# Kernel tuning notes

Measured on AMD Instinct MI355X. Metric: run time of the kernel, lower is better.

## Reference

```python
import jax, jax.numpy as jnp
import numpy as np

D_MODEL = 1024
NUM_HEADS = 16
DEPTH = D_MODEL // NUM_HEADS


def setup_inputs() -> dict:
    key = jax.random.key(0)
    ks = jax.random.split(key, 5)
    B, S = 2, 2048
    scale = 1.0 / np.sqrt(D_MODEL)
    x = jax.random.normal(ks[0], (B, S, D_MODEL), dtype=jnp.float32)
    wq = jax.random.normal(ks[1], (D_MODEL, D_MODEL), dtype=jnp.float32) * scale
    wk = jax.random.normal(ks[2], (D_MODEL, D_MODEL), dtype=jnp.float32) * scale
    wv = jax.random.normal(ks[3], (D_MODEL, D_MODEL), dtype=jnp.float32) * scale
    wo = jax.random.normal(ks[4], (D_MODEL, D_MODEL), dtype=jnp.float32) * scale
    zb = jnp.zeros((D_MODEL,), dtype=jnp.float32)
    return {"x": x, "wq": wq, "bq": zb, "wk": wk, "bk": zb, "wv": wv, "bv": zb, "wo": wo, "bo": zb}


def _split_heads(t):
    # [B, S, D] -> [B, H, S, depth]
    B, S, _ = t.shape
    return t.reshape(B, S, NUM_HEADS, DEPTH).transpose(0, 2, 1, 3)


def reference(x, wq, bq, wk, bk, wv, bv, wo, bo):
    q = _split_heads(x @ wq + bq)
    k = _split_heads(x @ wk + bk)
    v = _split_heads(x @ wv + bv)
    scores = jnp.einsum("bhqd,bhkd->bhqk", q, k) / jnp.sqrt(jnp.float32(DEPTH))
    attn = jax.nn.softmax(scores, axis=-1)
    out = jnp.einsum("bhqk,bhkd->bhqd", attn, v)  # [B, H, S, depth]
    B, H, S, d = out.shape
    out = out.transpose(0, 2, 1, 3).reshape(B, S, D_MODEL)
    return out @ wo + bo
```

## Files before the change

### kernel.cpp

```cpp
#include <hip/hip_runtime.h>
#include <stdint.h>

#define SS 2048
#define DM 1024
#define HD 16
#define DP 64
#define BB 2

#define QSCALE 0.18033688011112042f

typedef unsigned short u16;
typedef short bf16x8 __attribute__((ext_vector_type(8)));
typedef float f32x4 __attribute__((ext_vector_type(4)));

#if __has_builtin(__builtin_amdgcn_exp2f)
#define EXP2F __builtin_amdgcn_exp2f
#else
#define EXP2F exp2f
#endif

__device__ __forceinline__ u16 f2b(float f) {
  unsigned u = __builtin_bit_cast(unsigned, f);
  u = (u + 0x7fffu + ((u >> 16) & 1u)) >> 16;
  return (u16)u;
}

__device__ __forceinline__ void gl_lds16(const void* g, void* l) {
  __builtin_amdgcn_global_load_lds(
      (const __attribute__((address_space(1))) unsigned int*)g,
      (__attribute__((address_space(3))) unsigned int*)l, 16, 0, 0);
}

__global__ __launch_bounds__(256) void cast_bf16_kernel(const float* __restrict__ in,
                                                        u16* __restrict__ out, int n) {
  int i = (blockIdx.x * 256 + threadIdx.x) * 4;
  if (i + 3 < n) {
    float4 f = *reinterpret_cast<const float4*>(in + i);
    ushort4 o;
    o.x = f2b(f.x); o.y = f2b(f.y); o.z = f2b(f.z); o.w = f2b(f.w);
    *reinterpret_cast<ushort4*>(out + i) = o;
  }
}

__global__ __launch_bounds__(256) void tcast_kernel(const float* __restrict__ in,
                                                    u16* __restrict__ out, float scale) {
  __shared__ float tile[32][33];
  int tx = threadIdx.x & 31, ty = threadIdx.x >> 5;
  int c0 = blockIdx.x * 32;
  int r0 = blockIdx.y * 32;
#pragma unroll
  for (int j = 0; j < 4; ++j)
    tile[ty + j * 8][tx] = in[(size_t)(r0 + ty + j * 8) * DM + c0 + tx];
  __syncthreads();
#pragma unroll
  for (int j = 0; j < 4; ++j)
    out[(size_t)(c0 + ty + j * 8) * DM + r0 + tx] = f2b(tile[tx][ty + j * 8] * scale);
}

__global__ __launch_bounds__(256) void gemm_qkv(
    const u16* __restrict__ A, const u16* __restrict__ BT,
    const float* __restrict__ b0, const float* __restrict__ b1, const float* __restrict__ b2,
    u16* __restrict__ Oq, u16* __restrict__ Ok, u16* __restrict__ Ovt, int M, int K) {
  __shared__ __align__(16) u16 As[128][32];
  __shared__ __align__(16) u16 Bs[128][32];
  const int t = threadIdx.x;
  const int w = t >> 6, l = t & 63;
  const int lr = l & 15, lg = l >> 4;
  const int wr = w >> 1, wc = w & 1;
  const int m0 = blockIdx.y * 128, n0 = blockIdx.x * 128;

  const u16* Ab = A + (size_t)m0 * K;
  const u16* Bb = BT + (size_t)n0 * K;
  const int arow = t >> 2, achk = (t & 3) * 8;

  f32x4 acc[4][4];
#pragma unroll
  for (int mi = 0; mi < 4; ++mi)
#pragma unroll
    for (int ni = 0; ni < 4; ++ni)
      acc[mi][ni] = (f32x4){0.f, 0.f, 0.f, 0.f};

  char* AsB = (char*)(&As[0][0]);
  char* BsB = (char*)(&Bs[0][0]);

  for (int k0 = 0; k0 < K; k0 += 32) {
    gl_lds16(Ab + (size_t)arow * K + k0 + achk, AsB + t * 16);
    gl_lds16(Ab + (size_t)(arow + 64) * K + k0 + achk, AsB + t * 16 + 4096);
    gl_lds16(Bb + (size_t)arow * K + k0 + achk, BsB + t * 16);
    gl_lds16(Bb + (size_t)(arow + 64) * K + k0 + achk, BsB + t * 16 + 4096);
    __syncthreads();
    bf16x8 af[4], bfr[4];
#pragma unroll
    for (int mi = 0; mi < 4; ++mi)
      af[mi] = *(const bf16x8*)&As[wr * 64 + mi * 16 + lr][lg * 8];
#pragma unroll
    for (int ni = 0; ni < 4; ++ni)
      bfr[ni] = *(const bf16x8*)&Bs[wc * 64 + ni * 16 + lr][lg * 8];
#pragma unroll
    for (int mi = 0; mi < 4; ++mi)
#pragma unroll
      for (int ni = 0; ni < 4; ++ni)
        acc[mi][ni] =
            __builtin_amdgcn_mfma_f32_16x16x32_bf16(af[mi], bfr[ni], acc[mi][ni], 0, 0, 0);
    __syncthreads();
  }

  const int proj = n0 >> 10;
  const float* bias = proj == 0 ? b0 : (proj == 1 ? b1 : b2);
  const float bsc = proj == 0 ? QSCALE : 1.f;
  const int nloc0 = n0 & 1023;
#pragma unroll
  for (int mi = 0; mi < 4; ++mi)
#pragma unroll
    for (int ni = 0; ni < 4; ++ni)
#pragma unroll
      for (int i = 0; i < 4; ++i) {
        int gm = m0 + wr * 64 + mi * 16 + lg * 4 + i;
        int gn = nloc0 + wc * 64 + ni * 16 + lr;
        float vv = acc[mi][ni][i] + bias[gn] * bsc;
        int s = gm & (SS - 1), b = gm >> 11;
        int h = gn >> 6, d = gn & 63;
        if (proj == 2) {
          Ovt[(((size_t)(b * HD + h)) * DP + d) * SS + s] = f2b(vv);
        } else {
          u16* Op = proj == 0 ? Oq : Ok;
          Op[(((size_t)(b * HD + h)) * SS + s) * DP + d] = f2b(vv);
        }
      }
}

__global__ __launch_bounds__(256) void gemm_out(
    const u16* __restrict__ A, const u16* __restrict__ BT, const float* __restrict__ b0,
    float* __restrict__ FO, int M, int K) {
  __shared__ __align__(16) u16 As[64][64];
  __shared__ __align__(16) u16 Bs[64][64];
  const int t = threadIdx.x;
  const int w = t >> 6, l = t & 63;
  const int lr = l & 15, lg = l >> 4;
  const int wr = w >> 1, wc = w & 1;
  const int m0 = blockIdx.y * 64, n0 = blockIdx.x * 64;

  const u16* Ab = A + (size_t)m0 * K;
  const u16* Bb = BT + (size_t)n0 * K;
  const int srow = t >> 3;
  const int gchk = ((t & 7) ^ (srow & 7)) * 8;

  f32x4 acc[2][2];
#pragma unroll
  for (int mi = 0; mi < 2; ++mi)
#pragma unroll
    for (int ni = 0; ni < 2; ++ni)
      acc[mi][ni] = (f32x4){0.f, 0.f, 0.f, 0.f};

  char* AsB = (char*)(&As[0][0]);
  char* BsB = (char*)(&Bs[0][0]);

  for (int k0 = 0; k0 < K; k0 += 64) {
    gl_lds16(Ab + (size_t)srow * K + k0 + gchk, AsB + t * 16);
    gl_lds16(Ab + (size_t)(srow + 32) * K + k0 + gchk, AsB + t * 16 + 4096);
    gl_lds16(Bb + (size_t)srow * K + k0 + gchk, BsB + t * 16);
    gl_lds16(Bb + (size_t)(srow + 32) * K + k0 + gchk, BsB + t * 16 + 4096);
    __syncthreads();
    bf16x8 af[2][2], bfr[2][2];
#pragma unroll
    for (int mi = 0; mi < 2; ++mi) {
      int r = wr * 32 + mi * 16 + lr;
#pragma unroll
      for (int kk = 0; kk < 2; ++kk)
        af[mi][kk] = *(const bf16x8*)&As[r][(((kk * 4 + lg) ^ (r & 7)) * 8)];
    }
#pragma unroll
    for (int ni = 0; ni < 2; ++ni) {
      int r = wc * 32 + ni * 16 + lr;
#pragma unroll
      for (int kk = 0; kk < 2; ++kk)
        bfr[ni][kk] = *(const bf16x8*)&Bs[r][(((kk * 4 + lg) ^ (r & 7)) * 8)];
    }
#pragma unroll
    for (int mi = 0; mi < 2; ++mi)
#pragma unroll
      for (int ni = 0; ni < 2; ++ni)
#pragma unroll
        for (int kk = 0; kk < 2; ++kk)
          acc[mi][ni] =
              __builtin_amdgcn_mfma_f32_16x16x32_bf16(af[mi][kk], bfr[ni][kk], acc[mi][ni], 0, 0, 0);
    __syncthreads();
  }

#pragma unroll
  for (int mi = 0; mi < 2; ++mi)
#pragma unroll
    for (int ni = 0; ni < 2; ++ni)
#pragma unroll
      for (int i = 0; i < 4; ++i) {
        int gm = m0 + wr * 32 + mi * 16 + lg * 4 + i;
        int gn = n0 + wc * 32 + ni * 16 + lr;
        FO[(size_t)gm * DM + gn] = acc[mi][ni][i] + b0[gn];
      }
}

__global__ __launch_bounds__(256) void attn_kernel(const u16* __restrict__ Q,
                                                   const u16* __restrict__ K,
                                                   const u16* __restrict__ VT,
                                                   u16* __restrict__ O) {
  __shared__ __align__(16) u16 Ks[64 * 64];
  __shared__ __align__(16) u16 Vs[64 * 64];
  __shared__ __align__(16) u16 Ps[4][16][68];
  const int t = threadIdx.x, w = t >> 6, l = t & 63;
  const int lr = l & 15, lg = l >> 4;
  const int bh = blockIdx.y;
  const int q0 = blockIdx.x * 64;
  const u16* Qb = Q + (size_t)bh * SS * DP;
  const u16* Kb = K + (size_t)bh * SS * DP;
  const u16* Vb = VT + (size_t)bh * DP * SS;

  const int qrow = q0 + w * 16 + lr;
  bf16x8 qf[2];
  qf[0] = *(const bf16x8*)(Qb + (size_t)qrow * DP + lg * 8);
  qf[1] = *(const bf16x8*)(Qb + (size_t)qrow * DP + 32 + lg * 8);

  bf16x8 ones8;
#pragma unroll
  for (int j = 0; j < 8; ++j) ones8[j] = (short)0x3f80;

  f32x4 oacc[4];
  f32x4 lac = (f32x4){0.f, 0.f, 0.f, 0.f};
#pragma unroll
  for (int i = 0; i < 4; ++i) oacc[i] = (f32x4){0.f, 0.f, 0.f, 0.f};

  const int srow = t >> 3;
  const int sswz = ((t & 7) ^ (srow & 7)) * 8;
  char* KsB = (char*)Ks;
  char* VsB = (char*)Vs;

  for (int t0 = 0; t0 < SS; t0 += 64) {
    gl_lds16(Kb + (size_t)(t0 + srow) * DP + sswz, KsB + t * 16);
    gl_lds16(Kb + (size_t)(t0 + srow + 32) * DP + sswz, KsB + t * 16 + 4096);
    gl_lds16(Vb + (size_t)srow * SS + t0 + sswz, VsB + t * 16);
    gl_lds16(Vb + (size_t)(srow + 32) * SS + t0 + sswz, VsB + t * 16 + 4096);
    __syncthreads();

    f32x4 sc[4];
#pragma unroll
    for (int n = 0; n < 4; ++n) sc[n] = (f32x4){0.f, 0.f, 0.f, 0.f};
#pragma unroll
    for (int n = 0; n < 4; ++n) {
      int r = n * 16 + lr;
#pragma unroll
      for (int kk = 0; kk < 2; ++kk) {
        int chk = ((kk * 4 + lg) ^ (r & 7)) * 8;
        bf16x8 bk8 = *(const bf16x8*)(Ks + r * 64 + chk);
        sc[n] = __builtin_amdgcn_mfma_f32_16x16x32_bf16(qf[kk], bk8, sc[n], 0, 0, 0);
      }
    }

#pragma unroll
    for (int n = 0; n < 4; ++n)
#pragma unroll
      for (int i = 0; i < 4; ++i)
        Ps[w][lg * 4 + i][n * 16 + lr] = f2b(EXP2F(sc[n][i]));
    asm volatile("s_waitcnt lgkmcnt(0)" ::: "memory");
    bf16x8 pf[2];
    pf[0] = *(const bf16x8*)&Ps[w][lr][lg * 8];
    pf[1] = *(const bf16x8*)&Ps[w][lr][32 + lg * 8];

#pragma unroll
    for (int kk = 0; kk < 2; ++kk)
      lac = __builtin_amdgcn_mfma_f32_16x16x32_bf16(pf[kk], ones8, lac, 0, 0, 0);

#pragma unroll
    for (int n = 0; n < 4; ++n) {
      int r = n * 16 + lr;
#pragma unroll
      for (int kk = 0; kk < 2; ++kk) {
        int chk = ((kk * 4 + lg) ^ (r & 7)) * 8;
        bf16x8 bv8 = *(const bf16x8*)(Vs + r * 64 + chk);
        oacc[n] = __builtin_amdgcn_mfma_f32_16x16x32_bf16(pf[kk], bv8, oacc[n], 0, 0, 0);
      }
    }
    __syncthreads();
  }

  const int b = bh >> 4, h = bh & 15;
  float inv[4];
#pragma unroll
  for (int i = 0; i < 4; ++i) inv[i] = 1.0f / lac[i];
#pragma unroll
  for (int n = 0; n < 4; ++n)
#pragma unroll
    for (int i = 0; i < 4; ++i) {
      int row = q0 + w * 16 + lg * 4 + i;
      int col = h * 64 + n * 16 + lr;
      O[((size_t)(b * SS + row)) * DM + col] = f2b(oacc[n][i] * inv[i]);
    }
}

extern "C" void kernel_launch(void* const* d_in, const int* in_sizes, int n_in,
                              void* d_out, int out_size, void* d_ws, size_t ws_size,
                              hipStream_t stream) {
  const float* x = (const float*)d_in[0];
  const float* wq = (const float*)d_in[1];
  const float* bq = (const float*)d_in[2];
  const float* wk = (const float*)d_in[3];
  const float* bk = (const float*)d_in[4];
  const float* wv = (const float*)d_in[5];
  const float* bv = (const float*)d_in[6];
  const float* wo = (const float*)d_in[7];
  const float* bo = (const float*)d_in[8];
  float* out = (float*)d_out;

  u16* ws = (u16*)d_ws;
  u16* xb = ws;
  u16* wt3 = ws + 4194304;
  u16* wot = ws + 7340032;
  u16* q = ws + 8388608;
  u16* k = ws + 12582912;
  u16* vt = ws + 16777216;
  u16* o = ws;

  cast_bf16_kernel<<<4096, 256, 0, stream>>>(x, xb, 4194304);
  tcast_kernel<<<dim3(32, 32), 256, 0, stream>>>(wq, wt3, QSCALE);
  tcast_kernel<<<dim3(32, 32), 256, 0, stream>>>(wk, wt3 + 1048576, 1.f);
  tcast_kernel<<<dim3(32, 32), 256, 0, stream>>>(wv, wt3 + 2097152, 1.f);
  tcast_kernel<<<dim3(32, 32), 256, 0, stream>>>(wo, wot, 1.f);

  gemm_qkv<<<dim3(24, 32), 256, 0, stream>>>(xb, wt3, bq, bk, bv, q, k, vt, 4096, 1024);
  attn_kernel<<<dim3(32, 32), 256, 0, stream>>>(q, k, vt, o);
  gemm_out<<<dim3(16, 64), 256, 0, stream>>>(o, wot, bo, out, 4096, 1024);
}
```

Baseline: 220.0 us.

## Double-buffer attention K/V tiles, enlarge tiles, vectorize V stores, merge weight casts

The attention kernel now runs 512 threads per block over 128 query rows and double-buffers the K/V LDS tiles, so the next tile loads while the current one is computed and each K/V tile is shared by more query rows. The output GEMM moves to 128x64 tiles so each B fragment serves more rows. The QKV epilogue writes the transposed V output as packed 4-element stores instead of scalar stores. The four weight transpose-casts become a single launch. The risks are higher register and LDS pressure per block, fewer blocks for the output GEMM, and an explicit vmcnt wait each iteration that may limit how much loading overlaps with compute.

```diff
diff --git a/kernel.cpp b/kernel.cpp
--- a/kernel.cpp
+++ b/kernel.cpp
@@ -42,9 +42,15 @@
   }
 }
 
-__global__ __launch_bounds__(256) void tcast_kernel(const float* __restrict__ in,
-                                                    u16* __restrict__ out, float scale) {
+__global__ __launch_bounds__(256) void tcast4_kernel(
+    const float* __restrict__ w0, const float* __restrict__ w1,
+    const float* __restrict__ w2, const float* __restrict__ w3,
+    u16* __restrict__ o0, u16* __restrict__ o1, u16* __restrict__ o2, u16* __restrict__ o3) {
   __shared__ float tile[32][33];
+  const int z = blockIdx.z;
+  const float* in = z == 0 ? w0 : (z == 1 ? w1 : (z == 2 ? w2 : w3));
+  u16* out = z == 0 ? o0 : (z == 1 ? o1 : (z == 2 ? o2 : o3));
+  const float scale = z == 0 ? QSCALE : 1.f;
   int tx = threadIdx.x & 31, ty = threadIdx.x >> 5;
   int c0 = blockIdx.x * 32;
   int r0 = blockIdx.y * 32;
@@ -109,69 +115,85 @@
   const float* bias = proj == 0 ? b0 : (proj == 1 ? b1 : b2);
   const float bsc = proj == 0 ? QSCALE : 1.f;
   const int nloc0 = n0 & 1023;
-#pragma unroll
-  for (int mi = 0; mi < 4; ++mi)
-#pragma unroll
-    for (int ni = 0; ni < 4; ++ni)
-#pragma unroll
-      for (int i = 0; i < 4; ++i) {
-        int gm = m0 + wr * 64 + mi * 16 + lg * 4 + i;
+  if (proj == 2) {
+#pragma unroll
+    for (int mi = 0; mi < 4; ++mi)
+#pragma unroll
+      for (int ni = 0; ni < 4; ++ni) {
+        int gm0 = m0 + wr * 64 + mi * 16 + lg * 4;
         int gn = nloc0 + wc * 64 + ni * 16 + lr;
-        float vv = acc[mi][ni][i] + bias[gn] * bsc;
-        int s = gm & (SS - 1), b = gm >> 11;
+        int s0 = gm0 & (SS - 1), b = gm0 >> 11;
         int h = gn >> 6, d = gn & 63;
-        if (proj == 2) {
-          Ovt[(((size_t)(b * HD + h)) * DP + d) * SS + s] = f2b(vv);
-        } else {
-          u16* Op = proj == 0 ? Oq : Ok;
+        float bv = bias[gn];
+        ushort4 pk;
+        pk.x = f2b(acc[mi][ni][0] + bv);
+        pk.y = f2b(acc[mi][ni][1] + bv);
+        pk.z = f2b(acc[mi][ni][2] + bv);
+        pk.w = f2b(acc[mi][ni][3] + bv);
+        *reinterpret_cast<ushort4*>(Ovt + (((size_t)(b * HD + h)) * DP + d) * SS + s0) = pk;
+      }
+  } else {
+    u16* Op = proj == 0 ? Oq : Ok;
+#pragma unroll
+    for (int mi = 0; mi < 4; ++mi)
+#pragma unroll
+      for (int ni = 0; ni < 4; ++ni)
+#pragma unroll
+        for (int i = 0; i < 4; ++i) {
+          int gm = m0 + wr * 64 + mi * 16 + lg * 4 + i;
+          int gn = nloc0 + wc * 64 + ni * 16 + lr;
+          float vv = acc[mi][ni][i] + bias[gn] * bsc;
+          int s = gm & (SS - 1), b = gm >> 11;
+          int h = gn >> 6, d = gn & 63;
           Op[(((size_t)(b * HD + h)) * SS + s) * DP + d] = f2b(vv);
         }
-      }
+  }
 }
 
 __global__ __launch_bounds__(256) void gemm_out(
     const u16* __restrict__ A, const u16* __restrict__ BT, const float* __restrict__ b0,
     float* __restrict__ FO, int M, int K) {
-  __shared__ __align__(16) u16 As[64][64];
+  __shared__ __align__(16) u16 As[128][64];
   __shared__ __align__(16) u16 Bs[64][64];
   const int t = threadIdx.x;
   const int w = t >> 6, l = t & 63;
   const int lr = l & 15, lg = l >> 4;
-  const int wr = w >> 1, wc = w & 1;
-  const int m0 = blockIdx.y * 64, n0 = blockIdx.x * 64;
+  const int m0 = blockIdx.y * 128, n0 = blockIdx.x * 64;
 
   const u16* Ab = A + (size_t)m0 * K;
   const u16* Bb = BT + (size_t)n0 * K;
   const int srow = t >> 3;
-  const int gchk = ((t & 7) ^ (srow & 7)) * 8;
-
-  f32x4 acc[2][2];
+  const int schk = ((t & 7) ^ (srow & 7)) * 8;
+
+  f32x4 acc[2][4];
 #pragma unroll
   for (int mi = 0; mi < 2; ++mi)
 #pragma unroll
-    for (int ni = 0; ni < 2; ++ni)
+    for (int ni = 0; ni < 4; ++ni)
       acc[mi][ni] = (f32x4){0.f, 0.f, 0.f, 0.f};
 
   char* AsB = (char*)(&As[0][0]);
   char* BsB = (char*)(&Bs[0][0]);
 
   for (int k0 = 0; k0 < K; k0 += 64) {
-    gl_lds16(Ab + (size_t)srow * K + k0 + gchk, AsB + t * 16);
-    gl_lds16(Ab + (size_t)(srow + 32) * K + k0 + gchk, AsB + t * 16 + 4096);
-    gl_lds16(Bb + (size_t)srow * K + k0 + gchk, BsB + t * 16);
-    gl_lds16(Bb + (size_t)(srow + 32) * K + k0 + gchk, BsB + t * 16 + 4096);
-    __syncthreads();
-    bf16x8 af[2][2], bfr[2][2];
+#pragma unroll
+    for (int j = 0; j < 4; ++j)
+      gl_lds16(Ab + (size_t)(srow + 32 * j) * K + k0 + schk, AsB + t * 16 + j * 4096);
+#pragma unroll
+    for (int j = 0; j < 2; ++j)
+      gl_lds16(Bb + (size_t)(srow + 32 * j) * K + k0 + schk, BsB + t * 16 + j * 4096);
+    __syncthreads();
+    bf16x8 af[2][2], bfr[4][2];
 #pragma unroll
     for (int mi = 0; mi < 2; ++mi) {
-      int r = wr * 32 + mi * 16 + lr;
+      int r = w * 32 + mi * 16 + lr;
 #pragma unroll
       for (int kk = 0; kk < 2; ++kk)
         af[mi][kk] = *(const bf16x8*)&As[r][(((kk * 4 + lg) ^ (r & 7)) * 8)];
     }
 #pragma unroll
-    for (int ni = 0; ni < 2; ++ni) {
-      int r = wc * 32 + ni * 16 + lr;
+    for (int ni = 0; ni < 4; ++ni) {
+      int r = ni * 16 + lr;
 #pragma unroll
       for (int kk = 0; kk < 2; ++kk)
         bfr[ni][kk] = *(const bf16x8*)&Bs[r][(((kk * 4 + lg) ^ (r & 7)) * 8)];
@@ -179,7 +201,7 @@
 #pragma unroll
     for (int mi = 0; mi < 2; ++mi)
 #pragma unroll
-      for (int ni = 0; ni < 2; ++ni)
+      for (int ni = 0; ni < 4; ++ni)
 #pragma unroll
         for (int kk = 0; kk < 2; ++kk)
           acc[mi][ni] =
@@ -190,26 +212,26 @@
 #pragma unroll
   for (int mi = 0; mi < 2; ++mi)
 #pragma unroll
-    for (int ni = 0; ni < 2; ++ni)
+    for (int ni = 0; ni < 4; ++ni)
 #pragma unroll
       for (int i = 0; i < 4; ++i) {
-        int gm = m0 + wr * 32 + mi * 16 + lg * 4 + i;
-        int gn = n0 + wc * 32 + ni * 16 + lr;
+        int gm = m0 + w * 32 + mi * 16 + lg * 4 + i;
+        int gn = n0 + ni * 16 + lr;
         FO[(size_t)gm * DM + gn] = acc[mi][ni][i] + b0[gn];
       }
 }
 
-__global__ __launch_bounds__(256) void attn_kernel(const u16* __restrict__ Q,
+__global__ __launch_bounds__(512) void attn_kernel(const u16* __restrict__ Q,
                                                    const u16* __restrict__ K,
                                                    const u16* __restrict__ VT,
                                                    u16* __restrict__ O) {
-  __shared__ __align__(16) u16 Ks[64 * 64];
-  __shared__ __align__(16) u16 Vs[64 * 64];
-  __shared__ __align__(16) u16 Ps[4][16][68];
+  __shared__ __align__(16) u16 Ks[2][64 * 64];
+  __shared__ __align__(16) u16 Vs[2][64 * 64];
+  __shared__ __align__(16) u16 Ps[8][16][68];
   const int t = threadIdx.x, w = t >> 6, l = t & 63;
   const int lr = l & 15, lg = l >> 4;
   const int bh = blockIdx.y;
-  const int q0 = blockIdx.x * 64;
+  const int q0 = blockIdx.x * 128;
   const u16* Qb = Q + (size_t)bh * SS * DP;
   const u16* Kb = K + (size_t)bh * SS * DP;
   const u16* Vb = VT + (size_t)bh * DP * SS;
@@ -229,16 +251,21 @@
   for (int i = 0; i < 4; ++i) oacc[i] = (f32x4){0.f, 0.f, 0.f, 0.f};
 
   const int srow = t >> 3;
-  const int sswz = ((t & 7) ^ (srow & 7)) * 8;
-  char* KsB = (char*)Ks;
-  char* VsB = (char*)Vs;
-
-  for (int t0 = 0; t0 < SS; t0 += 64) {
-    gl_lds16(Kb + (size_t)(t0 + srow) * DP + sswz, KsB + t * 16);
-    gl_lds16(Kb + (size_t)(t0 + srow + 32) * DP + sswz, KsB + t * 16 + 4096);
-    gl_lds16(Vb + (size_t)srow * SS + t0 + sswz, VsB + t * 16);
-    gl_lds16(Vb + (size_t)(srow + 32) * SS + t0 + sswz, VsB + t * 16 + 4096);
-    __syncthreads();
+  const int schk = ((t & 7) ^ (srow & 7)) * 8;
+
+  gl_lds16(Kb + (size_t)srow * DP + schk, (char*)Ks[0] + t * 16);
+  gl_lds16(Vb + (size_t)srow * SS + 0 + schk, (char*)Vs[0] + t * 16);
+  asm volatile("s_waitcnt vmcnt(0)" ::: "memory");
+  __syncthreads();
+
+  int cur = 0;
+  for (int t0 = 0; t0 < SS; t0 += 64, cur ^= 1) {
+    if (t0 + 64 < SS) {
+      gl_lds16(Kb + (size_t)(t0 + 64 + srow) * DP + schk, (char*)Ks[cur ^ 1] + t * 16);
+      gl_lds16(Vb + (size_t)srow * SS + (t0 + 64) + schk, (char*)Vs[cur ^ 1] + t * 16);
+    }
+    const u16* Kc = Ks[cur];
+    const u16* Vc = Vs[cur];
 
     f32x4 sc[4];
 #pragma unroll
@@ -249,7 +276,7 @@
 #pragma unroll
       for (int kk = 0; kk < 2; ++kk) {
         int chk = ((kk * 4 + lg) ^ (r & 7)) * 8;
-        bf16x8 bk8 = *(const bf16x8*)(Ks + r * 64 + chk);
+        bf16x8 bk8 = *(const bf16x8*)(Kc + r * 64 + chk);
         sc[n] = __builtin_amdgcn_mfma_f32_16x16x32_bf16(qf[kk], bk8, sc[n], 0, 0, 0);
       }
     }
@@ -274,10 +301,11 @@
 #pragma unroll
       for (int kk = 0; kk < 2; ++kk) {
         int chk = ((kk * 4 + lg) ^ (r & 7)) * 8;
-        bf16x8 bv8 = *(const bf16x8*)(Vs + r * 64 + chk);
+        bf16x8 bv8 = *(const bf16x8*)(Vc + r * 64 + chk);
         oacc[n] = __builtin_amdgcn_mfma_f32_16x16x32_bf16(pf[kk], bv8, oacc[n], 0, 0, 0);
       }
     }
+    asm volatile("s_waitcnt vmcnt(0)" ::: "memory");
     __syncthreads();
   }
 
@@ -319,12 +347,10 @@
   u16* o = ws;
 
   cast_bf16_kernel<<<4096, 256, 0, stream>>>(x, xb, 4194304);
-  tcast_kernel<<<dim3(32, 32), 256, 0, stream>>>(wq, wt3, QSCALE);
-  tcast_kernel<<<dim3(32, 32), 256, 0, stream>>>(wk, wt3 + 1048576, 1.f);
-  tcast_kernel<<<dim3(32, 32), 256, 0, stream>>>(wv, wt3 + 2097152, 1.f);
-  tcast_kernel<<<dim3(32, 32), 256, 0, stream>>>(wo, wot, 1.f);
+  tcast4_kernel<<<dim3(32, 32, 4), 256, 0, stream>>>(wq, wk, wv, wo, wt3, wt3 + 1048576,
+                                                     wt3 + 2097152, wot);
 
   gemm_qkv<<<dim3(24, 32), 256, 0, stream>>>(xb, wt3, bq, bk, bv, q, k, vt, 4096, 1024);
-  attn_kernel<<<dim3(32, 32), 256, 0, stream>>>(q, k, vt, o);
-  gemm_out<<<dim3(16, 64), 256, 0, stream>>>(o, wot, bo, out, 4096, 1024);
-}
+  attn_kernel<<<dim3(16, 32), 512, 0, stream>>>(q, k, vt, o);
+  gemm_out<<<dim3(16, 32), 256, 0, stream>>>(o, wot, bo, out, 4096, 1024);
+}
```

Result: faster. 215.2 us (-2.2%).
